# Kernel optimization log

Measured on AMD Instinct MI355X. Metric: run time of the kernel, lower is better.

The kernel has to match this reference:

```python
import jax, jax.numpy as jnp
import numpy as np
from jax.scipy.special import logsumexp

B, N, D, NUM_CLASSES = 8192, 8192, 256, 64
TEMPERATURE = 1.0


def setup_inputs() -> dict:
    key = jax.random.key(0)
    k1, k2, k3, k4 = jax.random.split(key, 4)
    return {
        "text_features": jax.random.normal(k1, (B, D), dtype=jnp.float32),
        "image_features": jax.random.normal(k2, (N, D), dtype=jnp.float32),
        "t_label": jax.random.randint(k3, (B,), 0, NUM_CLASSES),
        "i_targets": jax.random.randint(k4, (N,), 0, NUM_CLASSES),
    }


def reference(text_features, image_features, t_label, i_targets):
    # logits[i,j] = <text_i, image_j> / T   -> [B, N]
    logits = jnp.matmul(text_features, image_features.T) / TEMPERATURE
    mask = t_label[:, None] == i_targets[None, :]  # [B, N] positives
    neg_inf = jnp.array(-jnp.inf, dtype=logits.dtype)
    # per-row logsumexp over positives of -logits, and over negatives of +logits
    lse_p = logsumexp(jnp.where(mask, -logits, neg_inf), axis=1)
    lse_n = logsumexp(jnp.where(mask, neg_inf, logits), axis=1)
    loss = jnp.mean(jax.nn.softplus(lse_n + lse_p))
    return loss
```

## Files before the change

### kernel.cpp

```cpp
#include <hip/hip_runtime.h>
#include <hip/hip_bf16.h>


#define B_ROWS   8192
#define N_COLS   8192
#define DIM      256
#define CSPLIT   32
#define NTILES   ((N_COLS / CSPLIT) / 32)
#define BLK_ROWS 128
#define THREADS  512

typedef __attribute__((ext_vector_type(8))) short bf16x8;
typedef __attribute__((ext_vector_type(4))) float f32x4;

#if __has_builtin(__builtin_amdgcn_exp2f)
#define EXP2F(x) __builtin_amdgcn_exp2f(x)
#else
#define EXP2F(x) exp2f(x)
#endif
#if __has_builtin(__builtin_amdgcn_logf)
#define LOG2F(x) __builtin_amdgcn_logf(x)
#else
#define LOG2F(x) log2f(x)
#endif

__device__ __forceinline__ unsigned short f2bf(float f) {
    union { float f; unsigned u; } c; c.f = f;
    return (unsigned short)((c.u + 0x7FFFu + ((c.u >> 16) & 1u)) >> 16);
}

__global__ void cvt_bf16_kernel(const float* __restrict__ in,
                                unsigned short* __restrict__ out, int n4) {
    int i = blockIdx.x * blockDim.x + threadIdx.x;
    if (i >= n4) return;
    float4 v = reinterpret_cast<const float4*>(in)[i];
    ushort4 o;
    o.x = f2bf(v.x); o.y = f2bf(v.y); o.z = f2bf(v.z); o.w = f2bf(v.w);
    reinterpret_cast<ushort4*>(out)[i] = o;
}

__global__ void cvt_bt_kernel(const float* __restrict__ img,
                              unsigned short* __restrict__ Bt) {
    int C = blockIdx.x * blockDim.x + threadIdx.x;
    if (C >= (N_COLS / 32) * 1024) return;
    int g = C >> 10, c = C & 1023;
    int col = g * 32 + (c & 31);
    int k8  = c >> 5;
    const float4* src =
        reinterpret_cast<const float4*>(img + (size_t)col * DIM + k8 * 8);
    float4 v0 = src[0], v1 = src[1];
    unsigned short s[8];
    s[0] = f2bf(v0.x); s[1] = f2bf(v0.y); s[2] = f2bf(v0.z); s[3] = f2bf(v0.w);
    s[4] = f2bf(v1.x); s[5] = f2bf(v1.y); s[6] = f2bf(v1.z); s[7] = f2bf(v1.w);
    reinterpret_cast<bf16x8*>(Bt)[C] = *reinterpret_cast<const bf16x8*>(s);
}

__launch_bounds__(THREADS, 4)
__global__ void fused_gemm_lse(const unsigned short* __restrict__ Abf,
                               const unsigned short* __restrict__ Bt,
                               const int* __restrict__ tlab,
                               const int* __restrict__ itgt,
                               float* __restrict__ gsum_p,
                               float* __restrict__ gsum_n) {
    __shared__ char lds[16384] __attribute__((aligned(128)));

    const int tid  = threadIdx.x;
    const int lane = tid & 63;
    const int wave = tid >> 6;
    const int l15  = lane & 15;
    const int q    = lane >> 4;
    const int rb   = blockIdx.x * BLK_ROWS + wave * 16;
    const int cb0  = blockIdx.y * (N_COLS / CSPLIT);

    bf16x8 afrag[8];
    const bf16x8* arow =
        reinterpret_cast<const bf16x8*>(Abf + (size_t)(rb + l15) * DIM) + q;
#pragma unroll
    for (int ks = 0; ks < 8; ++ks) afrag[ks] = arow[ks * 4];

    int rowcls[4];
#pragma unroll
    for (int j = 0; j < 4; ++j) rowcls[j] = tlab[rb + q * 4 + j];

    float sump[4] = {0.f, 0.f, 0.f, 0.f};
    float sumn[4] = {0.f, 0.f, 0.f, 0.f};

    const char* bsrc = (const char*)Bt
        + ((size_t)blockIdx.y * NTILES) * 16384 + tid * 16;
    char* ldsd = lds + tid * 16;

    const float L2E = 1.4426950408889634f;
    const float C2  = 72.0f;

    for (int t = 0; t < NTILES; ++t) {
#pragma unroll
        for (int i = 0; i < 2; ++i)
            __builtin_amdgcn_global_load_lds(
                (const __attribute__((address_space(1))) unsigned int*)
                    (bsrc + (size_t)t * 16384 + i * 8192),
                (__attribute__((address_space(3))) unsigned int*)
                    (ldsd + i * 8192),
                16, 0, 0);
        const int cc0 = itgt[cb0 + t * 32 + l15];
        const int cc1 = itgt[cb0 + t * 32 + 16 + l15];
        __syncthreads();

        f32x4 acc0 = {0.f, 0.f, 0.f, 0.f};
        f32x4 acc1 = {0.f, 0.f, 0.f, 0.f};
        const char* bb = lds + q * 512 + l15 * 16;
#pragma unroll
        for (int ks = 0; ks < 8; ++ks) {
            bf16x8 b0 = *reinterpret_cast<const bf16x8*>(bb + ks * 2048);
            bf16x8 b1 = *reinterpret_cast<const bf16x8*>(bb + ks * 2048 + 256);
            acc0 = __builtin_amdgcn_mfma_f32_16x16x32_bf16(afrag[ks], b0, acc0,
                                                           0, 0, 0);
            acc1 = __builtin_amdgcn_mfma_f32_16x16x32_bf16(afrag[ks], b1, acc1,
                                                           0, 0, 0);
        }
        __syncthreads();

#pragma unroll
        for (int j = 0; j < 4; ++j) {
            const float x0 = acc0[j];
            const bool  p0 = (rowcls[j] == cc0);
            const float e0 = EXP2F(__builtin_fmaf(x0, p0 ? -L2E : L2E, -C2));
            sump[j] += p0 ? e0 : 0.f;
            sumn[j] += p0 ? 0.f : e0;
            const float x1 = acc1[j];
            const bool  p1 = (rowcls[j] == cc1);
            const float e1 = EXP2F(__builtin_fmaf(x1, p1 ? -L2E : L2E, -C2));
            sump[j] += p1 ? e1 : 0.f;
            sumn[j] += p1 ? 0.f : e1;
        }
    }

#pragma unroll
    for (int j = 0; j < 4; ++j) {
        float vp = sump[j], vn = sumn[j];
#pragma unroll
        for (int m = 1; m < 16; m <<= 1) {
            vp += __shfl_xor(vp, m, 64);
            vn += __shfl_xor(vn, m, 64);
        }
        if (l15 == 0) {
            const int row = rb + q * 4 + j;
            atomicAdd(&gsum_p[row], vp);
            atomicAdd(&gsum_n[row], vn);
        }
    }
}

__global__ void finalize_kernel(const float* __restrict__ gsum_p,
                                const float* __restrict__ gsum_n,
                                float* __restrict__ out) {
    __shared__ float red[1024];
    const float LN2 = 0.6931471805599453f;
    const float C2  = 72.0f;
    float acc = 0.f;
    for (int i = threadIdx.x; i < B_ROWS; i += 1024) {
        float zp = (LOG2F(gsum_p[i]) + C2) * LN2;
        float zn = (LOG2F(gsum_n[i]) + C2) * LN2;
        float z  = zp + zn;
        float sp = fmaxf(z, 0.f) + log1pf(expf(-fabsf(z)));
        acc += sp;
    }
    red[threadIdx.x] = acc;
    __syncthreads();
    for (int s = 512; s > 0; s >>= 1) {
        if ((int)threadIdx.x < s) red[threadIdx.x] += red[threadIdx.x + s];
        __syncthreads();
    }
    if (threadIdx.x == 0) out[0] = red[0] / (float)B_ROWS;
}

extern "C" void kernel_launch(void* const* d_in, const int* in_sizes, int n_in,
                              void* d_out, int out_size, void* d_ws, size_t ws_size,
                              hipStream_t stream) {
    const float* text = (const float*)d_in[0];
    const float* img  = (const float*)d_in[1];
    const int* tlab   = (const int*)d_in[2];
    const int* itgt   = (const int*)d_in[3];
    float* out        = (float*)d_out;

    char* ws = (char*)d_ws;
    unsigned short* Abf = (unsigned short*)(ws);
    unsigned short* Bt  = (unsigned short*)(ws + (size_t)B_ROWS * DIM * 2);
    float* gsum_p = (float*)(ws + (size_t)(B_ROWS + N_COLS) * DIM * 2);
    float* gsum_n = gsum_p + B_ROWS;

    {
        int n4 = (B_ROWS * DIM) / 4;
        cvt_bf16_kernel<<<(n4 + 255) / 256, 256, 0, stream>>>(text, Abf, n4);
        int nc = (N_COLS / 32) * 1024;
        cvt_bt_kernel<<<(nc + 255) / 256, 256, 0, stream>>>(img, Bt);
    }

    hipMemsetAsync(gsum_p, 0, (size_t)(B_ROWS * 2) * sizeof(float), stream);

    dim3 grid(B_ROWS / BLK_ROWS, CSPLIT);
    fused_gemm_lse<<<grid, THREADS, 0, stream>>>(Abf, Bt, tlab, itgt,
                                                 gsum_p, gsum_n);

    finalize_kernel<<<1, 1024, 0, stream>>>(gsum_p, gsum_n, out);
}
```

Baseline: 74.21 us.

## Double-buffer B tiles in LDS and fuse conversion kernels with zeroing

```diff
diff --git a/kernel.cpp b/kernel.cpp
--- a/kernel.cpp
+++ b/kernel.cpp
@@ -29,30 +29,35 @@
     return (unsigned short)((c.u + 0x7FFFu + ((c.u >> 16) & 1u)) >> 16);
 }
 
-__global__ void cvt_bf16_kernel(const float* __restrict__ in,
-                                unsigned short* __restrict__ out, int n4) {
-    int i = blockIdx.x * blockDim.x + threadIdx.x;
-    if (i >= n4) return;
-    float4 v = reinterpret_cast<const float4*>(in)[i];
-    ushort4 o;
-    o.x = f2bf(v.x); o.y = f2bf(v.y); o.z = f2bf(v.z); o.w = f2bf(v.w);
-    reinterpret_cast<ushort4*>(out)[i] = o;
-}
-
-__global__ void cvt_bt_kernel(const float* __restrict__ img,
-                              unsigned short* __restrict__ Bt) {
-    int C = blockIdx.x * blockDim.x + threadIdx.x;
-    if (C >= (N_COLS / 32) * 1024) return;
-    int g = C >> 10, c = C & 1023;
-    int col = g * 32 + (c & 31);
-    int k8  = c >> 5;
-    const float4* src =
-        reinterpret_cast<const float4*>(img + (size_t)col * DIM + k8 * 8);
-    float4 v0 = src[0], v1 = src[1];
-    unsigned short s[8];
-    s[0] = f2bf(v0.x); s[1] = f2bf(v0.y); s[2] = f2bf(v0.z); s[3] = f2bf(v0.w);
-    s[4] = f2bf(v1.x); s[5] = f2bf(v1.y); s[6] = f2bf(v1.z); s[7] = f2bf(v1.w);
-    reinterpret_cast<bf16x8*>(Bt)[C] = *reinterpret_cast<const bf16x8*>(s);
+__global__ void cvt_all_kernel(const float* __restrict__ text,
+                               const float* __restrict__ img,
+                               unsigned short* __restrict__ Abf,
+                               unsigned short* __restrict__ Bt,
+                               float* __restrict__ gsum) {
+    const int i = blockIdx.x * blockDim.x + threadIdx.x;
+    if (i < 4096) {
+        reinterpret_cast<float4*>(gsum)[i] = float4{0.f, 0.f, 0.f, 0.f};
+    }
+    if (i < 262144) {
+        const float4* src = reinterpret_cast<const float4*>(text) + i * 2;
+        float4 v0 = src[0], v1 = src[1];
+        unsigned short s[8];
+        s[0] = f2bf(v0.x); s[1] = f2bf(v0.y); s[2] = f2bf(v0.z); s[3] = f2bf(v0.w);
+        s[4] = f2bf(v1.x); s[5] = f2bf(v1.y); s[6] = f2bf(v1.z); s[7] = f2bf(v1.w);
+        reinterpret_cast<bf16x8*>(Abf)[i] = *reinterpret_cast<const bf16x8*>(s);
+    } else {
+        const int C = i - 262144;
+        const int g = C >> 10, c = C & 1023;
+        const int col = g * 32 + (c & 31);
+        const int k8  = c >> 5;
+        const float4* src =
+            reinterpret_cast<const float4*>(img + (size_t)col * DIM + k8 * 8);
+        float4 v0 = src[0], v1 = src[1];
+        unsigned short s[8];
+        s[0] = f2bf(v0.x); s[1] = f2bf(v0.y); s[2] = f2bf(v0.z); s[3] = f2bf(v0.w);
+        s[4] = f2bf(v1.x); s[5] = f2bf(v1.y); s[6] = f2bf(v1.z); s[7] = f2bf(v1.w);
+        reinterpret_cast<bf16x8*>(Bt)[C] = *reinterpret_cast<const bf16x8*>(s);
+    }
 }
 
 __launch_bounds__(THREADS, 4)
@@ -62,7 +67,7 @@
                                const int* __restrict__ itgt,
                                float* __restrict__ gsum_p,
                                float* __restrict__ gsum_n) {
-    __shared__ char lds[16384] __attribute__((aligned(128)));
+    __shared__ char lds[2 * 16384] __attribute__((aligned(128)));
 
     const int tid  = threadIdx.x;
     const int lane = tid & 63;
@@ -82,6 +87,13 @@
 #pragma unroll
     for (int j = 0; j < 4; ++j) rowcls[j] = tlab[rb + q * 4 + j];
 
+    int ccls0[NTILES], ccls1[NTILES];
+#pragma unroll
+    for (int t = 0; t < NTILES; ++t) {
+        ccls0[t] = itgt[cb0 + t * 32 + l15];
+        ccls1[t] = itgt[cb0 + t * 32 + 16 + l15];
+    }
+
     float sump[4] = {0.f, 0.f, 0.f, 0.f};
     float sumn[4] = {0.f, 0.f, 0.f, 0.f};
 
@@ -89,25 +101,36 @@
         + ((size_t)blockIdx.y * NTILES) * 16384 + tid * 16;
     char* ldsd = lds + tid * 16;
 
+#define STAGE(T, BUF) do {                                                    \
+    _Pragma("unroll")                                                         \
+    for (int i_ = 0; i_ < 2; ++i_)                                            \
+        __builtin_amdgcn_global_load_lds(                                     \
+            (const __attribute__((address_space(1))) unsigned int*)           \
+                (bsrc + (size_t)(T) * 16384 + i_ * 8192),                     \
+            (__attribute__((address_space(3))) unsigned int*)                 \
+                (ldsd + (BUF) * 16384 + i_ * 8192),                           \
+            16, 0, 0);                                                        \
+} while (0)
+
     const float L2E = 1.4426950408889634f;
     const float C2  = 72.0f;
 
+    STAGE(0, 0);
+
+#pragma unroll
     for (int t = 0; t < NTILES; ++t) {
-#pragma unroll
-        for (int i = 0; i < 2; ++i)
-            __builtin_amdgcn_global_load_lds(
-                (const __attribute__((address_space(1))) unsigned int*)
-                    (bsrc + (size_t)t * 16384 + i * 8192),
-                (__attribute__((address_space(3))) unsigned int*)
-                    (ldsd + i * 8192),
-                16, 0, 0);
-        const int cc0 = itgt[cb0 + t * 32 + l15];
-        const int cc1 = itgt[cb0 + t * 32 + 16 + l15];
-        __syncthreads();
+        if (t + 1 < NTILES) {
+            STAGE(t + 1, (t + 1) & 1);
+            asm volatile("s_waitcnt vmcnt(2)" ::: "memory");
+        } else {
+            asm volatile("s_waitcnt vmcnt(0)" ::: "memory");
+        }
+        __builtin_amdgcn_s_barrier();
+        __builtin_amdgcn_sched_barrier(0);
 
         f32x4 acc0 = {0.f, 0.f, 0.f, 0.f};
         f32x4 acc1 = {0.f, 0.f, 0.f, 0.f};
-        const char* bb = lds + q * 512 + l15 * 16;
+        const char* bb = lds + (t & 1) * 16384 + q * 512 + l15 * 16;
 #pragma unroll
         for (int ks = 0; ks < 8; ++ks) {
             bf16x8 b0 = *reinterpret_cast<const bf16x8*>(bb + ks * 2048);
@@ -117,8 +140,10 @@
             acc1 = __builtin_amdgcn_mfma_f32_16x16x32_bf16(afrag[ks], b1, acc1,
                                                            0, 0, 0);
         }
-        __syncthreads();
-
+        __builtin_amdgcn_sched_barrier(0);
+        __builtin_amdgcn_s_barrier();
+
+        const int cc0 = ccls0[t], cc1 = ccls1[t];
 #pragma unroll
         for (int j = 0; j < 4; ++j) {
             const float x0 = acc0[j];
@@ -133,6 +158,7 @@
             sumn[j] += p1 ? 0.f : e1;
         }
     }
+#undef STAGE
 
 #pragma unroll
     for (int j = 0; j < 4; ++j) {
@@ -188,14 +214,8 @@
     float* gsum_p = (float*)(ws + (size_t)(B_ROWS + N_COLS) * DIM * 2);
     float* gsum_n = gsum_p + B_ROWS;
 
-    {
-        int n4 = (B_ROWS * DIM) / 4;
-        cvt_bf16_kernel<<<(n4 + 255) / 256, 256, 0, stream>>>(text, Abf, n4);
-        int nc = (N_COLS / 32) * 1024;
-        cvt_bt_kernel<<<(nc + 255) / 256, 256, 0, stream>>>(img, Bt);
-    }
-
-    hipMemsetAsync(gsum_p, 0, (size_t)(B_ROWS * 2) * sizeof(float), stream);
+    cvt_all_kernel<<<(2 * 262144) / 256, 256, 0, stream>>>(text, img, Abf, Bt,
+                                                           gsum_p);
 
     dim3 grid(B_ROWS / BLK_ROWS, CSPLIT);
     fused_gemm_lse<<<grid, THREADS, 0, stream>>>(Abf, Bt, tlab, itgt,
```

New measurement: 70.95 us. 1.05x faster.
